# Performance work log

Measured on AMD Instinct MI355X. Metric: run time of the kernel, lower is better.

## Reference

```python
import jax, jax.numpy as jnp
import numpy as np

V_PATCH = (1, 2, 4, 8, 16, 32)
RESI = 0.5   # abs(quant_resi)
BETA = 0.25
K_PHI = 4    # share_quant_resi


def _phi_idx(si, SN, K=K_PHI):
    # PhiPartiallyShared.__getitem__ with at = si/(SN-1)
    ticks = np.linspace(1/3/K, 1 - 1/3/K, K) if K == 4 else np.linspace(1/2/K, 1 - 1/2/K, K)
    return int(np.argmin(np.abs(ticks - si / (SN - 1))))


def _area_down(x, pn):
    # F.interpolate mode='area' with pn | H  == exact block mean
    B, C, H, W = x.shape
    return x.reshape(B, C, pn, H // pn, pn, W // pn).mean(axis=(3, 5))


def _bilinear(x, size):
    # matches torch bilinear, align_corners=False, antialias=False (half-pixel centers)
    B, C, _, _ = x.shape
    return jax.image.resize(x, (B, C, size, size), method='bilinear', antialias=False)


def _down(x, pn, si):
    if pn == x.shape[2]:
        return x
    return _area_down(x, pn) if si <= 3 else _bilinear(x, pn)


def _phi_ada(h, w, b, fw, fb, sn):
    # Phi_ada: conv weight modulated by fc(SN); fc is zero-init but kept in the graph
    C = h.shape[1]
    cond = (fw[:, 0] * jnp.float32(sn) + fb).reshape(C, C, 1, 1)
    wmod = w * (1.0 + cond)
    y = jax.lax.conv_general_dilated(h, wmod, (1, 1), 'SAME',
                                     dimension_numbers=('NCHW', 'OIHW', 'NCHW'))
    y = y + b[None, :, None, None]
    return h * (1.0 - RESI) + y * RESI


def _forward(f, embed_w, conv_w, conv_b, fc_w, fc_b):
    B, C, H, W = f.shape
    SN = len(V_PATCH)
    f_ng = jax.lax.stop_gradient(f)
    f_rest = f_ng
    f_hat = jnp.zeros_like(f_ng)
    e_ng = jax.lax.stop_gradient(embed_w)            # embedding.weight.data
    e_sq = jnp.sum(e_ng * e_ng, axis=1)              # [V]
    vq_losses = []
    commit = jnp.float32(0.0)
    for si, pn in enumerate(V_PATCH):
        rest = f_rest if si == SN - 1 else _down(f_rest, pn, si)
        rest_NC = rest.transpose(0, 2, 3, 1).reshape(-1, C)          # [N,C]
        # squared L2 distances to codebook, argmin (non-differentiable)
        d = (jnp.sum(rest_NC * rest_NC, axis=1, keepdims=True)
             + e_sq - 2.0 * (rest_NC @ e_ng.T))                       # [N,V]
        idx = jnp.argmin(d, axis=1)                                   # [N]
        h = embed_w[idx].reshape(B, pn, pn, C).transpose(0, 3, 1, 2)  # [B,C,pn,pn]
        if si != SN - 1:
            h = _bilinear(h, H)
        k = _phi_idx(si, SN)
        h = _phi_ada(h, conv_w[k], conv_b[k], fc_w[k], fc_b[k], SN)
        f_hat = f_hat + h
        f_rest = f_rest - jax.lax.stop_gradient(h)    # grad through f_rest is killed by argmin anyway
        vq_losses.append(jnp.mean((f_hat - f_ng) ** 2))
        fh_ng = jax.lax.stop_gradient(f_hat)
        commit = commit + jnp.mean((_down(fh_ng, pn, si) - _down(f, pn, si)) ** 2) * BETA
    commit = commit / SN
    # straight-through estimator
    f_hat_out = jax.lax.stop_gradient(f_hat) - f_ng + f
    return f_hat_out, jnp.stack(vq_losses), commit


def setup_inputs() -> dict:
    key = jax.random.key(0)
    k1, k2, k3 = jax.random.split(key, 3)
    B, C, H, W = 32, 64, 32, 32
    V = 4096
    f_BChw = jax.random.normal(k1, (B, C, H, W), dtype=jnp.float32)
    embed_w = jax.random.normal(k2, (V, C), dtype=jnp.float32) * 0.5  # trunc_normal std=0.5
    conv_w = jax.random.normal(k3, (K_PHI, C, C, 3, 3), dtype=jnp.float32) * 0.02
    conv_b = jnp.zeros((K_PHI, C), dtype=jnp.float32)
    fc_w = jnp.zeros((K_PHI, C * C, 1), dtype=jnp.float32)  # Phi_ada.fc zero-init
    fc_b = jnp.zeros((K_PHI, C * C), dtype=jnp.float32)
    return {'f_BChw': f_BChw, 'embed_w': embed_w, 'conv_w': conv_w,
            'conv_b': conv_b, 'fc_w': fc_w, 'fc_b': fc_b}


def reference(f_BChw, embed_w, conv_w, conv_b, fc_w, fc_b):
    return _forward(f_BChw, embed_w, conv_w, conv_b, fc_w, fc_b)
```

## Files before the change

### kernel.cpp

```cpp
#include <hip/hip_runtime.h>
#include <cfloat>

#define N_ELEM 2097152
#define TAU 2.0e-2f

typedef short s16x8 __attribute__((ext_vector_type(8)));
typedef float f32x4 __attribute__((ext_vector_type(4)));

__device__ __forceinline__ unsigned short f2bf(float v) {
    unsigned u = __float_as_uint(v);
    u += 0x7FFFu + ((u >> 16) & 1u);
    return (unsigned short)(u >> 16);
}
__device__ __forceinline__ float bf2f(unsigned short h) {
    return __uint_as_float(((unsigned)h) << 16);
}

__device__ __forceinline__ float blockReduceSum(float v) {
    __shared__ float red[4];
    #pragma unroll
    for (int off = 32; off; off >>= 1) v += __shfl_down(v, off, 64);
    int wid = threadIdx.x >> 6, lane = threadIdx.x & 63;
    if (lane == 0) red[wid] = v;
    __syncthreads();
    float r = 0.f;
    if (threadIdx.x == 0) {
        int nw = ((int)blockDim.x + 63) >> 6;
        for (int w = 0; w < nw; ++w) r += red[w];
    }
    __syncthreads();
    return r;
}

__global__ void k_embprep(const float* __restrict__ e, float* __restrict__ hesq,
                          unsigned short* __restrict__ ehiN, unsigned short* __restrict__ eloN) {
    int v = blockIdx.x * 256 + threadIdx.x;
    if (v >= 4096) return;
    const float4* r = (const float4*)(e + (size_t)v * 64);
    float s = 0.f;
    #pragma unroll
    for (int i = 0; i < 16; ++i) {
        float4 a = r[i];
        s += a.x * a.x + a.y * a.y + a.z * a.z + a.w * a.w;
    }
    hesq[v] = 0.5f * s;
    for (int i = 0; i < 64; ++i) {
        float x = e[(size_t)v * 64 + i];
        unsigned short h = f2bf(x);
        ehiN[(size_t)v * 64 + i] = h ^ 0x8000u;
        eloN[(size_t)v * 64 + i] = f2bf(x - bf2f(h)) ^ 0x8000u;
    }
}

__global__ void k_wmod(const float* __restrict__ w, const float* __restrict__ fcw,
                       const float* __restrict__ fcb,
                       unsigned short* __restrict__ wh, unsigned short* __restrict__ wl) {
    int i = blockIdx.x * 256 + threadIdx.x;
    if (i >= 4 * 64 * 64 * 9) return;
    int k = i / (64 * 64 * 9);
    int r = i % (64 * 64 * 9);
    int oi = r / 9;
    int t = r % 9;
    int co = oi >> 6, ci = oi & 63;
    float cond = fcw[k * 4096 + oi] * 6.0f + fcb[k * 4096 + oi];
    float v = w[i] * (1.0f + cond);
    size_t o = ((size_t)(k * 9 + t) * 64 + co) * 64 + ci;
    unsigned short h = f2bf(v);
    wh[o] = h;
    wl[o] = f2bf(v - bf2f(h));
}

__global__ __launch_bounds__(256) void k_down_plane(
        const float* __restrict__ f, const float* __restrict__ fhat,
        float* __restrict__ restnc, unsigned short* __restrict__ dhi,
        unsigned short* __restrict__ dlo, float* __restrict__ cmpPrev, int pn) {
    __shared__ float hs[32][16];
    __shared__ float cr[32][16];
    __shared__ float pm[256];
    int bc = blockIdx.x;
    int c = bc & 63, b = bc >> 6;
    int t = threadIdx.x;
    const float4* fp = (const float4*)(f + (size_t)bc * 1024);
    const float4* hp = (const float4*)(fhat + (size_t)bc * 1024);
    float4 a = fp[t], q = hp[t];
    int r = t >> 3, c4 = t & 7;
    hs[r][c4 * 2]     = (a.x - q.x) + (a.y - q.y);
    hs[r][c4 * 2 + 1] = (a.z - q.z) + (a.w - q.w);
    __syncthreads();
    int cpp = 16 / pn;
    for (int i = t; i < 32 * pn; i += 256) {
        int rr = i / pn, px = i % pn;
        float s = 0.f;
        for (int j = 0; j < cpp; ++j) s += hs[rr][px * cpp + j];
        cr[rr][px] = s;
    }
    __syncthreads();
    int s_ = 32 / pn;
    float inv = 1.0f / (float)(s_ * s_);
    for (int p = t; p < pn * pn; p += 256) {
        int py = p / pn, px = p % pn;
        float s = 0.f;
        for (int j = 0; j < s_; ++j) s += cr[py * s_ + j][px];
        float m = s * inv;
        pm[p] = m;
        int n = (b * pn + py) * pn + px;
        size_t o = (size_t)n * 64 + c;
        unsigned short h = f2bf(m);
        restnc[o] = m;
        dhi[o] = h;
        dlo[o] = f2bf(m - bf2f(h));
    }
    if (pn >= 2) {
        __syncthreads();
        int pnp = pn >> 1;
        float m2 = 0.f;
        for (int p = t; p < pnp * pnp; p += 256) {
            int py = p / pnp, px = p % pnp;
            float mm = 0.25f * (pm[(2 * py) * pn + 2 * px] + pm[(2 * py) * pn + 2 * px + 1]
                              + pm[(2 * py + 1) * pn + 2 * px] + pm[(2 * py + 1) * pn + 2 * px + 1]);
            m2 += mm * mm;
        }
        m2 = blockReduceSum(m2);
        if (t == 0) cmpPrev[blockIdx.x] = m2;
    }
}

__global__ void k_trans_nc(const float* __restrict__ A, const float* __restrict__ Bt,
                           float* __restrict__ dst,
                           unsigned short* __restrict__ dhi, unsigned short* __restrict__ dlo,
                           float* __restrict__ cmp) {
    __shared__ float t[64][65];
    int b = blockIdx.x;
    int p0 = blockIdx.y * 64;
    int lane = threadIdx.x & 63, r4 = threadIdx.x >> 6;
    #pragma unroll
    for (int i = 0; i < 16; ++i) {
        int c = i * 4 + r4;
        size_t g = ((size_t)b * 64 + c) * 1024 + p0 + lane;
        t[c][lane] = A[g] - Bt[g];
    }
    __syncthreads();
    #pragma unroll
    for (int i = 0; i < 16; ++i) {
        int p = i * 4 + r4;
        size_t o = ((size_t)(b * 1024 + p0 + p)) * 64 + lane;
        float v = t[lane][p];
        unsigned short h = f2bf(v);
        dst[o] = v;
        dhi[o] = h;
        dlo[o] = f2bf(v - bf2f(h));
    }
    float m2s = 0.f;
    for (int i = threadIdx.x; i < 1024; i += 256) {
        int c = i & 63, px = i >> 6;
        float m = 0.25f * (t[c][2 * px] + t[c][2 * px + 1] + t[c][32 + 2 * px] + t[c][33 + 2 * px]);
        m2s += m * m;
    }
    m2s = blockReduceSum(m2s);
    if (threadIdx.x == 0) cmp[blockIdx.x * 16 + blockIdx.y] = m2s;
}

__global__ __launch_bounds__(256) void k_vq_mfma(
        const unsigned short* __restrict__ resthi, const unsigned short* __restrict__ restlo,
        const unsigned short* __restrict__ embhiN, const unsigned short* __restrict__ embloN,
        const float* __restrict__ hesq,
        float* __restrict__ m1v_, int* __restrict__ m1i_, float* __restrict__ m2v_,
        int N, int CPS) {
    __shared__ __align__(16) unsigned short lah[64 * 64];
    __shared__ __align__(16) unsigned short lal[64 * 64];
    __shared__ __align__(16) float lq[64];
    int tid = threadIdx.x;
    int lane = tid & 63, wv = tid >> 6;
    int split = blockIdx.y;
    int p0 = blockIdx.x * 128 + wv * 32;
    int cr = lane & 15, oct = lane >> 4;
    int ko8 = oct * 8;
    int ptA = p0 + cr, ptB = p0 + 16 + cr;
    int pA = min(ptA, N - 1), pB = min(ptB, N - 1);

    const unsigned short* ra = resthi + (size_t)pA * 64;
    const unsigned short* la = restlo + (size_t)pA * 64;
    const unsigned short* rb = resthi + (size_t)pB * 64;
    const unsigned short* lb = restlo + (size_t)pB * 64;
    s16x8 bhA0 = *(const s16x8*)(ra + ko8);
    s16x8 bhA1 = *(const s16x8*)(ra + 32 + ko8);
    s16x8 blA0 = *(const s16x8*)(la + ko8);
    s16x8 blA1 = *(const s16x8*)(la + 32 + ko8);
    s16x8 bhB0 = *(const s16x8*)(rb + ko8);
    s16x8 bhB1 = *(const s16x8*)(rb + 32 + ko8);
    s16x8 blB0 = *(const s16x8*)(lb + ko8);
    s16x8 blB1 = *(const s16x8*)(lb + 32 + ko8);

    float m1vA = FLT_MAX, m2vA = FLT_MAX; int m1iA = 0;
    float m1vB = FLT_MAX, m2vB = FLT_MAX; int m1iB = 0;
    int sw = (cr & 7) << 4;

    int cbeg = split * CPS;
    for (int oc = 0; oc < CPS; oc += 64) {
        int cb = cbeg + oc;
        __syncthreads();
        for (int t = tid; t < 512; t += 256) {
            int cc = t >> 3, part = t & 7;
            int bo = (cc * 128 + part * 16) ^ ((cc & 7) << 4);
            *(uint4*)((char*)lah + bo) = *(const uint4*)(embhiN + (size_t)(cb + cc) * 64 + part * 8);
            *(uint4*)((char*)lal + bo) = *(const uint4*)(embloN + (size_t)(cb + cc) * 64 + part * 8);
        }
        if (tid < 64) lq[tid] = hesq[cb + tid];
        __syncthreads();
        #pragma unroll
        for (int sub = 0; sub < 4; ++sub) {
            int rowb = (sub * 16 + cr) * 128;
            s16x8 ah0 = *(const s16x8*)((const char*)lah + ((rowb + ko8 * 2) ^ sw));
            s16x8 ah1 = *(const s16x8*)((const char*)lah + ((rowb + 64 + ko8 * 2) ^ sw));
            s16x8 al0 = *(const s16x8*)((const char*)lal + ((rowb + ko8 * 2) ^ sw));
            s16x8 al1 = *(const s16x8*)((const char*)lal + ((rowb + 64 + ko8 * 2) ^ sw));
            f32x4 q = *(const f32x4*)(lq + sub * 16 + oct * 4);
            int crow = cb + sub * 16 + oct * 4;
            f32x4 acc = q;
            acc = __builtin_amdgcn_mfma_f32_16x16x32_bf16(ah0, bhA0, acc, 0, 0, 0);
            acc = __builtin_amdgcn_mfma_f32_16x16x32_bf16(ah1, bhA1, acc, 0, 0, 0);
            acc = __builtin_amdgcn_mfma_f32_16x16x32_bf16(ah0, blA0, acc, 0, 0, 0);
            acc = __builtin_amdgcn_mfma_f32_16x16x32_bf16(ah1, blA1, acc, 0, 0, 0);
            acc = __builtin_amdgcn_mfma_f32_16x16x32_bf16(al0, bhA0, acc, 0, 0, 0);
            acc = __builtin_amdgcn_mfma_f32_16x16x32_bf16(al1, bhA1, acc, 0, 0, 0);
            #pragma unroll
            for (int r = 0; r < 4; ++r) {
                float s = acc[r];
                bool lt = s < m1vA;
                m2vA = fminf(fmaxf(s, m1vA), m2vA);
                m1iA = lt ? (crow + r) : m1iA;
                m1vA = fminf(s, m1vA);
            }
            f32x4 accB = q;
            accB = __builtin_amdgcn_mfma_f32_16x16x32_bf16(ah0, bhB0, accB, 0, 0, 0);
            accB = __builtin_amdgcn_mfma_f32_16x16x32_bf16(ah1, bhB1, accB, 0, 0, 0);
            accB = __builtin_amdgcn_mfma_f32_16x16x32_bf16(ah0, blB0, accB, 0, 0, 0);
            accB = __builtin_amdgcn_mfma_f32_16x16x32_bf16(ah1, blB1, accB, 0, 0, 0);
            accB = __builtin_amdgcn_mfma_f32_16x16x32_bf16(al0, bhB0, accB, 0, 0, 0);
            accB = __builtin_amdgcn_mfma_f32_16x16x32_bf16(al1, bhB1, accB, 0, 0, 0);
            #pragma unroll
            for (int r = 0; r < 4; ++r) {
                float s = accB[r];
                bool lt = s < m1vB;
                m2vB = fminf(fmaxf(s, m1vB), m2vB);
                m1iB = lt ? (crow + r) : m1iB;
                m1vB = fminf(s, m1vB);
            }
        }
    }
    #pragma unroll
    for (int off = 16; off <= 32; off <<= 1) {
        float o1 = __shfl_xor(m1vA, off, 64); int oi = __shfl_xor(m1iA, off, 64);
        float o2 = __shfl_xor(m2vA, off, 64);
        bool lt = o1 < m1vA;
        m2vA = fminf(fmaxf(o1, m1vA), fminf(m2vA, o2));
        m1vA = fminf(o1, m1vA);
        m1iA = lt ? oi : m1iA;
        o1 = __shfl_xor(m1vB, off, 64); oi = __shfl_xor(m1iB, off, 64);
        o2 = __shfl_xor(m2vB, off, 64);
        lt = o1 < m1vB;
        m2vB = fminf(fmaxf(o1, m1vB), fminf(m2vB, o2));
        m1vB = fminf(o1, m1vB);
        m1iB = lt ? oi : m1iB;
    }
    if (oct == 0) {
        if (ptA < N) { size_t o = (size_t)split * N + ptA; m1v_[o] = m1vA; m1i_[o] = m1iA; m2v_[o] = m2vA; }
        if (ptB < N) { size_t o = (size_t)split * N + ptB; m1v_[o] = m1vB; m1i_[o] = m1iB; m2v_[o] = m2vB; }
    }
}

__global__ void k_vq_combine(const float* __restrict__ m1v_, const int* __restrict__ m1i_,
                             const float* __restrict__ m2v_,
                             int* __restrict__ idx, int* __restrict__ flag, int* __restrict__ count,
                             unsigned long long* __restrict__ pmin, int N, int SPLITS) {
    int n = blockIdx.x * 256 + threadIdx.x;
    if (n >= N) return;
    float a1v = m1v_[n], a2v = m2v_[n];
    int a1i = m1i_[n];
    for (int s = 1; s < SPLITS; ++s) {
        size_t o = (size_t)s * N + n;
        float b1v = m1v_[o], b2v = m2v_[o];
        int b1i = m1i_[o];
        bool lt = b1v < a1v;
        a2v = fminf(fmaxf(b1v, a1v), fminf(a2v, b2v));
        a1v = fminf(b1v, a1v);
        a1i = lt ? b1i : a1i;
    }
    idx[n] = a1i;
    pmin[n] = 0xFFFFFFFFFFFFFFFFull;
    if (a2v - a1v < TAU) {
        int p = atomicAdd(count, 1);
        flag[p] = n;
    }
}

__global__ __launch_bounds__(256) void k_vq_exact(
        const float* __restrict__ restnc, const float* __restrict__ embed,
        const float* __restrict__ hesq, const int* __restrict__ flag,
        const int* __restrict__ count, unsigned long long* __restrict__ pmin) {
    __shared__ float rs[32 * 64];
    int tid = threadIdx.x;
    int lane = tid & 63;
    int cnt = *count;
    int nb = (cnt + 31) >> 5;
    int ntask = nb * 16;
    for (int task = blockIdx.x; task < ntask; task += gridDim.x) {
        int batch = task >> 4, spl = task & 15;
        int lbase = batch << 5;
        int npts = min(32, cnt - lbase);
        __syncthreads();
        for (int i = tid; i < npts * 64; i += 256) {
            int li = i >> 6;
            rs[i] = restnc[(size_t)flag[lbase + li] * 64 + (i & 63)];
        }
        __syncthreads();
        int code = spl * 256 + tid;
        const float4* e4 = (const float4*)(embed + (size_t)code * 64);
        float4 e[16];
        #pragma unroll
        for (int i = 0; i < 16; ++i) e[i] = e4[i];
        float hq = hesq[code];
        for (int p = 0; p < npts; ++p) {
            const float4* r4 = (const float4*)(rs + p * 64);
            float d0 = 0.f, d1 = 0.f, d2 = 0.f, d3 = 0.f;
            #pragma unroll
            for (int i = 0; i < 16; i += 4) {
                float4 e0 = e[i], e1 = e[i + 1], e2 = e[i + 2], e3 = e[i + 3];
                d0 += e0.x * r4[i].x     + e0.y * r4[i].y     + e0.z * r4[i].z     + e0.w * r4[i].w;
                d1 += e1.x * r4[i + 1].x + e1.y * r4[i + 1].y + e1.z * r4[i + 1].z + e1.w * r4[i + 1].w;
                d2 += e2.x * r4[i + 2].x + e2.y * r4[i + 2].y + e2.z * r4[i + 2].z + e2.w * r4[i + 2].w;
                d3 += e3.x * r4[i + 3].x + e3.y * r4[i + 3].y + e3.z * r4[i + 3].z + e3.w * r4[i + 3].w;
            }
            float s = hq - ((d0 + d1) + (d2 + d3));
            unsigned u = __float_as_uint(s);
            u = (u & 0x80000000u) ? ~u : (u | 0x80000000u);
            unsigned long long pk = (((unsigned long long)u) << 32) | (unsigned)code;
            #pragma unroll
            for (int off = 32; off; off >>= 1) {
                unsigned long long o = __shfl_down(pk, off, 64);
                if (o < pk) pk = o;
            }
            if (lane == 0) atomicMin(pmin + flag[lbase + p], pk);
        }
    }
}

__global__ __launch_bounds__(256) void k_conv_mfma(
        const int* __restrict__ idx, const unsigned long long* __restrict__ pmin,
        const float* __restrict__ embed,
        const unsigned short* __restrict__ wh, const unsigned short* __restrict__ wl,
        const float* __restrict__ bias, const float* __restrict__ f_in,
        float* __restrict__ f_hat, float* __restrict__ vq_part, int pn) {
    __shared__ __align__(16) unsigned short Xh[4 * 34 * 64];
    __shared__ __align__(16) unsigned short Xl[4 * 34 * 64];
    __shared__ int pid[136][4];
    __shared__ float pwt[136][2];
    int b = blockIdx.x, rg = blockIdx.y;
    int y0 = rg * 2;
    int tid = threadIdx.x;
    int lane = tid & 63, wv = tid >> 6;
    int coh = (wv & 1) * 32;
    int ph  = (wv >> 1) * 2;
    int cr = lane & 15, oct = lane >> 4;

    if (tid < 136) {
        int lr = tid / 34, lc = tid % 34;
        int gy = y0 + lr - 1, gx = lc - 1;
        if (gy >= 0 && gy < 32 && gx >= 0 && gx < 32) {
            if (pn == 32) {
                int n = (b * 32 + gy) * 32 + gx;
                unsigned long long pv = pmin[n];
                int id = (pv != 0xFFFFFFFFFFFFFFFFull) ? (int)(pv & 0xFFFFFFFFull) : idx[n];
                pid[tid][0] = id; pid[tid][1] = id; pid[tid][2] = id; pid[tid][3] = id;
                pwt[tid][0] = 0.f; pwt[tid][1] = 0.f;
            } else {
                float scale = (float)pn * (1.0f / 32.0f);
                float sy = (gy + 0.5f) * scale - 0.5f;
                float sx = (gx + 0.5f) * scale - 0.5f;
                float fy0 = floorf(sy), fx0 = floorf(sx);
                float wy = sy - fy0, wx = sx - fx0;
                int yy0 = max(0, min(pn - 1, (int)fy0));
                int yy1 = max(0, min(pn - 1, (int)fy0 + 1));
                int xx0 = max(0, min(pn - 1, (int)fx0));
                int xx1 = max(0, min(pn - 1, (int)fx0 + 1));
                int nb_ = b * pn * pn;
                int n00 = nb_ + yy0 * pn + xx0, n01 = nb_ + yy0 * pn + xx1;
                int n10 = nb_ + yy1 * pn + xx0, n11 = nb_ + yy1 * pn + xx1;
                unsigned long long p00 = pmin[n00], p01 = pmin[n01];
                unsigned long long p10 = pmin[n10], p11 = pmin[n11];
                pid[tid][0] = (p00 != 0xFFFFFFFFFFFFFFFFull) ? (int)(p00 & 0xFFFFFFFFull) : idx[n00];
                pid[tid][1] = (p01 != 0xFFFFFFFFFFFFFFFFull) ? (int)(p01 & 0xFFFFFFFFull) : idx[n01];
                pid[tid][2] = (p10 != 0xFFFFFFFFFFFFFFFFull) ? (int)(p10 & 0xFFFFFFFFull) : idx[n10];
                pid[tid][3] = (p11 != 0xFFFFFFFFFFFFFFFFull) ? (int)(p11 & 0xFFFFFFFFull) : idx[n11];
                pwt[tid][0] = wy; pwt[tid][1] = wx;
            }
        } else {
            pid[tid][0] = -1;
        }
    }
    __syncthreads();

    for (int q = tid; q < 136 * 8; q += 256) {
        int pl = q >> 3, o8 = q & 7;
        int lc = pl % 34;
        int bo = (pl * 128 + o8 * 16) ^ ((lc & 7) << 4);
        uint4 vh = {0, 0, 0, 0}, vl = {0, 0, 0, 0};
        int i00 = pid[pl][0];
        if (i00 >= 0) {
            int i01 = pid[pl][1], i10 = pid[pl][2], i11 = pid[pl][3];
            float wy = pwt[pl][0], wx = pwt[pl][1];
            const float4* e00 = (const float4*)(embed + (size_t)i00 * 64 + o8 * 8);
            const float4* e01 = (const float4*)(embed + (size_t)i01 * 64 + o8 * 8);
            const float4* e10 = (const float4*)(embed + (size_t)i10 * 64 + o8 * 8);
            const float4* e11 = (const float4*)(embed + (size_t)i11 * 64 + o8 * 8);
            union { unsigned short u[8]; uint4 v; } oh, ol;
            #pragma unroll
            for (int half = 0; half < 2; ++half) {
                float4 a00 = e00[half], a01 = e01[half], a10 = e10[half], a11 = e11[half];
                float vv[4];
                vv[0] = (a00.x + wx * (a01.x - a00.x)) + wy * ((a10.x + wx * (a11.x - a10.x)) - (a00.x + wx * (a01.x - a00.x)));
                vv[1] = (a00.y + wx * (a01.y - a00.y)) + wy * ((a10.y + wx * (a11.y - a10.y)) - (a00.y + wx * (a01.y - a00.y)));
                vv[2] = (a00.z + wx * (a01.z - a00.z)) + wy * ((a10.z + wx * (a11.z - a10.z)) - (a00.z + wx * (a01.z - a00.z)));
                vv[3] = (a00.w + wx * (a01.w - a00.w)) + wy * ((a10.w + wx * (a11.w - a10.w)) - (a00.w + wx * (a01.w - a00.w)));
                #pragma unroll
                for (int j = 0; j < 4; ++j) {
                    unsigned short h = f2bf(vv[j]);
                    oh.u[half * 4 + j] = h;
                    ol.u[half * 4 + j] = f2bf(vv[j] - bf2f(h));
                }
            }
            vh = oh.v; vl = ol.v;
        }
        *(uint4*)((char*)Xh + bo) = vh;
        *(uint4*)((char*)Xl + bo) = vl;
    }
    __syncthreads();

    f32x4 acc[2][2];
    #pragma unroll
    for (int ct = 0; ct < 2; ++ct)
        #pragma unroll
        for (int pp = 0; pp < 2; ++pp) acc[ct][pp] = (f32x4){0.f, 0.f, 0.f, 0.f};

    for (int t = 0; t < 9; ++t) {
        int dy = t / 3, dx = t % 3;
        #pragma unroll
        for (int cc = 0; cc < 2; ++cc) {
            size_t wo0 = ((size_t)t * 64 + coh + cr) * 64 + cc * 32 + oct * 8;
            size_t wo1 = ((size_t)t * 64 + coh + 16 + cr) * 64 + cc * 32 + oct * 8;
            s16x8 Ah0 = *(const s16x8*)(wh + wo0);
            s16x8 Al0 = *(const s16x8*)(wl + wo0);
            s16x8 Ah1 = *(const s16x8*)(wh + wo1);
            s16x8 Al1 = *(const s16x8*)(wl + wo1);
            #pragma unroll
            for (int pp = 0; pp < 2; ++pp) {
                int px = (ph + pp) * 16 + cr;
                int lr = (px >> 5) + dy;
                int lc = (px & 31) + dx;
                int bo = ((lr * 34 + lc) * 128 + cc * 64 + oct * 16) ^ ((lc & 7) << 4);
                s16x8 Bh = *(const s16x8*)((const char*)Xh + bo);
                s16x8 Bl = *(const s16x8*)((const char*)Xl + bo);
                acc[0][pp] = __builtin_amdgcn_mfma_f32_16x16x32_bf16(Ah0, Bh, acc[0][pp], 0, 0, 0);
                acc[0][pp] = __builtin_amdgcn_mfma_f32_16x16x32_bf16(Ah0, Bl, acc[0][pp], 0, 0, 0);
                acc[0][pp] = __builtin_amdgcn_mfma_f32_16x16x32_bf16(Al0, Bh, acc[0][pp], 0, 0, 0);
                acc[1][pp] = __builtin_amdgcn_mfma_f32_16x16x32_bf16(Ah1, Bh, acc[1][pp], 0, 0, 0);
                acc[1][pp] = __builtin_amdgcn_mfma_f32_16x16x32_bf16(Ah1, Bl, acc[1][pp], 0, 0, 0);
                acc[1][pp] = __builtin_amdgcn_mfma_f32_16x16x32_bf16(Al1, Bh, acc[1][pp], 0, 0, 0);
            }
        }
    }

    float local = 0.f;
    #pragma unroll
    for (int ct = 0; ct < 2; ++ct) {
        int cbase = coh + ct * 16 + oct * 4;
        #pragma unroll
        for (int pp = 0; pp < 2; ++pp) {
            int px = (ph + pp) * 16 + cr;
            int y = y0 + (px >> 5), x = px & 31;
            int lr = (px >> 5) + 1, lc = (px & 31) + 1;
            int bo = ((lr * 34 + lc) * 128 + cbase * 2) ^ ((lc & 7) << 4);
            ushort4 hvh = *(const ushort4*)((const char*)Xh + bo);
            ushort4 hvl = *(const ushort4*)((const char*)Xl + bo);
            #pragma unroll
            for (int r = 0; r < 4; ++r) {
                int co = cbase + r;
                unsigned short uh = (r == 0) ? hvh.x : (r == 1) ? hvh.y : (r == 2) ? hvh.z : hvh.w;
                unsigned short ul = (r == 0) ? hvl.x : (r == 1) ? hvl.y : (r == 2) ? hvl.z : hvl.w;
                float hv = bf2f(uh) + bf2f(ul);
                float hconv = acc[ct][pp][r] + bias[co];
                float hout = 0.5f * hv + 0.5f * hconv;
                size_t o = (((size_t)(b * 64 + co)) * 32 + y) * 32 + x;
                float fh = f_hat[o] + hout;
                f_hat[o] = fh;
                float d = fh - f_in[o];
                local += d * d;
            }
        }
    }
    local = blockReduceSum(local);
    if (tid == 0) vq_part[b * 16 + rg] = local;
}

__global__ void k_final(const float* __restrict__ vqp, const float* __restrict__ cmpP,
                        float* __restrict__ out) {
    const int pn2s[5] = {1, 4, 16, 64, 256};
    const int slots[5] = {2048, 2048, 2048, 2048, 512};
    __shared__ float commit_s;
    if (threadIdx.x == 0) commit_s = 0.f;
    __syncthreads();
    for (int si = 0; si < 6; ++si) {
        float l = vqp[si * 512 + threadIdx.x] + vqp[si * 512 + 256 + threadIdx.x];
        l = blockReduceSum(l);
        if (threadIdx.x == 0) {
            float vl = l / (float)N_ELEM;
            out[N_ELEM + si] = vl;
            if (si == 5) commit_s += vl * 0.25f;
        }
        if (si < 5) {
            float csum = 0.f;
            for (int i = threadIdx.x; i < slots[si]; i += 256) csum += cmpP[si * 2048 + i];
            csum = blockReduceSum(csum);
            if (threadIdx.x == 0) commit_s += csum / (float)(2048 * pn2s[si]) * 0.25f;
        }
    }
    __syncthreads();
    if (threadIdx.x == 0) out[N_ELEM + 6] = commit_s / 6.0f;
}

extern "C" void kernel_launch(void* const* d_in, const int* in_sizes, int n_in,
                              void* d_out, int out_size, void* d_ws, size_t ws_size,
                              hipStream_t stream) {
    const float* f     = (const float*)d_in[0];
    const float* embed = (const float*)d_in[1];
    const float* convw = (const float*)d_in[2];
    const float* convb = (const float*)d_in[3];
    const float* fcw   = (const float*)d_in[4];
    const float* fcb   = (const float*)d_in[5];
    float* out = (float*)d_out;
    float* ws  = (float*)d_ws;

    float* restnc = ws + 2097152;
    unsigned short* resthi = (unsigned short*)(ws + 4194304);
    unsigned short* restlo = (unsigned short*)(ws + 5242880);
    unsigned short* embhiN = (unsigned short*)(ws + 6291456);
    unsigned short* embloN = (unsigned short*)(ws + 6422528);
    unsigned short* wmodh  = (unsigned short*)(ws + 6553600);
    unsigned short* wmodl  = (unsigned short*)(ws + 6627328);
    float* hesq   = ws + 6701056;
    float* m1v    = ws + 6705152;
    float* m2v    = ws + 6967296;
    int*   m1i    = (int*)(ws + 7229440);
    int*   idx    = (int*)(ws + 7491584);
    int*   flag   = (int*)(ws + 7524352);
    int*   count  = (int*)(ws + 7557120);
    unsigned long long* pmin = (unsigned long long*)(ws + 7557184);
    float* vqp    = ws + 7622720;
    float* cmpP   = ws + 7625792;

    hipMemsetAsync(d_out, 0, (size_t)out_size * sizeof(float), stream);
    hipMemsetAsync(count, 0, 6 * sizeof(int), stream);
    k_wmod<<<576, 256, 0, stream>>>(convw, fcw, fcb, wmodh, wmodl);
    k_embprep<<<16, 256, 0, stream>>>(embed, hesq, embhiN, embloN);

    const int pns[6]    = {1, 2, 4, 8, 16, 32};
    const int splits[6] = {64, 64, 64, 64, 16, 8};
    const int kidx[6]   = {0, 0, 1, 2, 3, 3};

    for (int si = 0; si < 6; ++si) {
        int pn = pns[si], pn2 = pn * pn;
        int N = 32 * pn2, SPL = splits[si], CPS = 4096 / SPL;

        if (si <= 4) {
            k_down_plane<<<2048, 256, 0, stream>>>(f, out, restnc, resthi, restlo,
                                                   si >= 1 ? cmpP + (si - 1) * 2048 : nullptr, pn);
        } else {
            k_trans_nc<<<dim3(32, 16), 256, 0, stream>>>(f, out, restnc, resthi, restlo,
                                                         cmpP + 4 * 2048);
        }

        k_vq_mfma<<<dim3((N + 127) / 128, SPL), 256, 0, stream>>>(resthi, restlo, embhiN, embloN, hesq,
                                                                  m1v, m1i, m2v, N, CPS);
        k_vq_combine<<<(N + 255) / 256, 256, 0, stream>>>(m1v, m1i, m2v, idx, flag, count + si, pmin, N, SPL);
        k_vq_exact<<<512, 256, 0, stream>>>(restnc, embed, hesq, flag, count + si, pmin);

        k_conv_mfma<<<dim3(32, 16), 256, 0, stream>>>(idx, pmin, embed,
                                                      wmodh + kidx[si] * 36864, wmodl + kidx[si] * 36864,
                                                      convb + kidx[si] * 64, f, out, vqp + si * 512, pn);
    }

    k_final<<<1, 256, 0, stream>>>(vqp, cmpP, out);
}
```

Baseline: 609.9 us.

## Enlarge conv tile to four rows per block and fold count reset into prep

The conv kernel now processes four output rows per block with 512 threads and a six-row halo tile instead of two rows with 256 threads. This halves the halo overhead and halves the block count. The pn==32 path skips the redundant four-way bilinear gather, and the count memset is folded into k_embprep to save a launch. The wave-to-row mapping must extend to eight waves. The larger LDS footprint and block size may reduce occupancy.

```diff
diff --git a/kernel.cpp b/kernel.cpp
--- a/kernel.cpp
+++ b/kernel.cpp
@@ -17,7 +17,7 @@
 }
 
 __device__ __forceinline__ float blockReduceSum(float v) {
-    __shared__ float red[4];
+    __shared__ float red[8];
     #pragma unroll
     for (int off = 32; off; off >>= 1) v += __shfl_down(v, off, 64);
     int wid = threadIdx.x >> 6, lane = threadIdx.x & 63;
@@ -33,7 +33,9 @@
 }
 
 __global__ void k_embprep(const float* __restrict__ e, float* __restrict__ hesq,
-                          unsigned short* __restrict__ ehiN, unsigned short* __restrict__ eloN) {
+                          unsigned short* __restrict__ ehiN, unsigned short* __restrict__ eloN,
+                          int* __restrict__ count) {
+    if (blockIdx.x == 0 && threadIdx.x < 6) count[threadIdx.x] = 0;
     int v = blockIdx.x * 256 + threadIdx.x;
     if (v >= 4096) return;
     const float4* r = (const float4*)(e + (size_t)v * 64);
@@ -345,25 +347,25 @@
     }
 }
 
-__global__ __launch_bounds__(256) void k_conv_mfma(
+__global__ __launch_bounds__(512) void k_conv_mfma(
         const int* __restrict__ idx, const unsigned long long* __restrict__ pmin,
         const float* __restrict__ embed,
         const unsigned short* __restrict__ wh, const unsigned short* __restrict__ wl,
         const float* __restrict__ bias, const float* __restrict__ f_in,
         float* __restrict__ f_hat, float* __restrict__ vq_part, int pn) {
-    __shared__ __align__(16) unsigned short Xh[4 * 34 * 64];
-    __shared__ __align__(16) unsigned short Xl[4 * 34 * 64];
-    __shared__ int pid[136][4];
-    __shared__ float pwt[136][2];
+    __shared__ __align__(16) unsigned short Xh[6 * 34 * 64];
+    __shared__ __align__(16) unsigned short Xl[6 * 34 * 64];
+    __shared__ int pid[204][4];
+    __shared__ float pwt[204][2];
     int b = blockIdx.x, rg = blockIdx.y;
-    int y0 = rg * 2;
+    int y0 = rg * 4;
     int tid = threadIdx.x;
     int lane = tid & 63, wv = tid >> 6;
     int coh = (wv & 1) * 32;
     int ph  = (wv >> 1) * 2;
     int cr = lane & 15, oct = lane >> 4;
 
-    if (tid < 136) {
+    if (tid < 204) {
         int lr = tid / 34, lc = tid % 34;
         int gy = y0 + lr - 1, gx = lc - 1;
         if (gy >= 0 && gy < 32 && gx >= 0 && gx < 32) {
@@ -371,8 +373,7 @@
                 int n = (b * 32 + gy) * 32 + gx;
                 unsigned long long pv = pmin[n];
                 int id = (pv != 0xFFFFFFFFFFFFFFFFull) ? (int)(pv & 0xFFFFFFFFull) : idx[n];
-                pid[tid][0] = id; pid[tid][1] = id; pid[tid][2] = id; pid[tid][3] = id;
-                pwt[tid][0] = 0.f; pwt[tid][1] = 0.f;
+                pid[tid][0] = id;
             } else {
                 float scale = (float)pn * (1.0f / 32.0f);
                 float sy = (gy + 0.5f) * scale - 0.5f;
@@ -400,33 +401,48 @@
     }
     __syncthreads();
 
-    for (int q = tid; q < 136 * 8; q += 256) {
+    for (int q = tid; q < 204 * 8; q += 512) {
         int pl = q >> 3, o8 = q & 7;
         int lc = pl % 34;
         int bo = (pl * 128 + o8 * 16) ^ ((lc & 7) << 4);
         uint4 vh = {0, 0, 0, 0}, vl = {0, 0, 0, 0};
         int i00 = pid[pl][0];
         if (i00 >= 0) {
-            int i01 = pid[pl][1], i10 = pid[pl][2], i11 = pid[pl][3];
-            float wy = pwt[pl][0], wx = pwt[pl][1];
-            const float4* e00 = (const float4*)(embed + (size_t)i00 * 64 + o8 * 8);
-            const float4* e01 = (const float4*)(embed + (size_t)i01 * 64 + o8 * 8);
-            const float4* e10 = (const float4*)(embed + (size_t)i10 * 64 + o8 * 8);
-            const float4* e11 = (const float4*)(embed + (size_t)i11 * 64 + o8 * 8);
             union { unsigned short u[8]; uint4 v; } oh, ol;
-            #pragma unroll
-            for (int half = 0; half < 2; ++half) {
-                float4 a00 = e00[half], a01 = e01[half], a10 = e10[half], a11 = e11[half];
-                float vv[4];
-                vv[0] = (a00.x + wx * (a01.x - a00.x)) + wy * ((a10.x + wx * (a11.x - a10.x)) - (a00.x + wx * (a01.x - a00.x)));
-                vv[1] = (a00.y + wx * (a01.y - a00.y)) + wy * ((a10.y + wx * (a11.y - a10.y)) - (a00.y + wx * (a01.y - a00.y)));
-                vv[2] = (a00.z + wx * (a01.z - a00.z)) + wy * ((a10.z + wx * (a11.z - a10.z)) - (a00.z + wx * (a01.z - a00.z)));
-                vv[3] = (a00.w + wx * (a01.w - a00.w)) + wy * ((a10.w + wx * (a11.w - a10.w)) - (a00.w + wx * (a01.w - a00.w)));
+            if (pn == 32) {
+                const float4* e00 = (const float4*)(embed + (size_t)i00 * 64 + o8 * 8);
                 #pragma unroll
-                for (int j = 0; j < 4; ++j) {
-                    unsigned short h = f2bf(vv[j]);
-                    oh.u[half * 4 + j] = h;
-                    ol.u[half * 4 + j] = f2bf(vv[j] - bf2f(h));
+                for (int half = 0; half < 2; ++half) {
+                    float4 a00 = e00[half];
+                    float vv[4] = {a00.x, a00.y, a00.z, a00.w};
+                    #pragma unroll
+                    for (int j = 0; j < 4; ++j) {
+                        unsigned short h = f2bf(vv[j]);
+                        oh.u[half * 4 + j] = h;
+                        ol.u[half * 4 + j] = f2bf(vv[j] - bf2f(h));
+                    }
+                }
+            } else {
+                int i01 = pid[pl][1], i10 = pid[pl][2], i11 = pid[pl][3];
+                float wy = pwt[pl][0], wx = pwt[pl][1];
+                const float4* e00 = (const float4*)(embed + (size_t)i00 * 64 + o8 * 8);
+                const float4* e01 = (const float4*)(embed + (size_t)i01 * 64 + o8 * 8);
+                const float4* e10 = (const float4*)(embed + (size_t)i10 * 64 + o8 * 8);
+                const float4* e11 = (const float4*)(embed + (size_t)i11 * 64 + o8 * 8);
+                #pragma unroll
+                for (int half = 0; half < 2; ++half) {
+                    float4 a00 = e00[half], a01 = e01[half], a10 = e10[half], a11 = e11[half];
+                    float t0, t1, vv[4];
+                    t0 = a00.x + wx * (a01.x - a00.x); t1 = a10.x + wx * (a11.x - a10.x); vv[0] = t0 + wy * (t1 - t0);
+                    t0 = a00.y + wx * (a01.y - a00.y); t1 = a10.y + wx * (a11.y - a10.y); vv[1] = t0 + wy * (t1 - t0);
+                    t0 = a00.z + wx * (a01.z - a00.z); t1 = a10.z + wx * (a11.z - a10.z); vv[2] = t0 + wy * (t1 - t0);
+                    t0 = a00.w + wx * (a01.w - a00.w); t1 = a10.w + wx * (a11.w - a10.w); vv[3] = t0 + wy * (t1 - t0);
+                    #pragma unroll
+                    for (int j = 0; j < 4; ++j) {
+                        unsigned short h = f2bf(vv[j]);
+                        oh.u[half * 4 + j] = h;
+                        ol.u[half * 4 + j] = f2bf(vv[j] - bf2f(h));
+                    }
                 }
             }
             vh = oh.v; vl = ol.v;
@@ -499,7 +515,7 @@
         }
     }
     local = blockReduceSum(local);
-    if (tid == 0) vq_part[b * 16 + rg] = local;
+    if (tid == 0) vq_part[b * 8 + rg] = local;
 }
 
 __global__ void k_final(const float* __restrict__ vqp, const float* __restrict__ cmpP,
@@ -510,7 +526,7 @@
     if (threadIdx.x == 0) commit_s = 0.f;
     __syncthreads();
     for (int si = 0; si < 6; ++si) {
-        float l = vqp[si * 512 + threadIdx.x] + vqp[si * 512 + 256 + threadIdx.x];
+        float l = vqp[si * 256 + threadIdx.x];
         l = blockReduceSum(l);
         if (threadIdx.x == 0) {
             float vl = l / (float)N_ELEM;
@@ -556,12 +572,11 @@
     int*   count  = (int*)(ws + 7557120);
     unsigned long long* pmin = (unsigned long long*)(ws + 7557184);
     float* vqp    = ws + 7622720;
-    float* cmpP   = ws + 7625792;
+    float* cmpP   = ws + 7624256;
 
     hipMemsetAsync(d_out, 0, (size_t)out_size * sizeof(float), stream);
-    hipMemsetAsync(count, 0, 6 * sizeof(int), stream);
     k_wmod<<<576, 256, 0, stream>>>(convw, fcw, fcb, wmodh, wmodl);
-    k_embprep<<<16, 256, 0, stream>>>(embed, hesq, embhiN, embloN);
+    k_embprep<<<16, 256, 0, stream>>>(embed, hesq, embhiN, embloN, count);
 
     const int pns[6]    = {1, 2, 4, 8, 16, 32};
     const int splits[6] = {64, 64, 64, 64, 16, 8};
@@ -584,9 +599,9 @@
         k_vq_combine<<<(N + 255) / 256, 256, 0, stream>>>(m1v, m1i, m2v, idx, flag, count + si, pmin, N, SPL);
         k_vq_exact<<<512, 256, 0, stream>>>(restnc, embed, hesq, flag, count + si, pmin);
 
-        k_conv_mfma<<<dim3(32, 16), 256, 0, stream>>>(idx, pmin, embed,
-                                                      wmodh + kidx[si] * 36864, wmodl + kidx[si] * 36864,
-                                                      convb + kidx[si] * 64, f, out, vqp + si * 512, pn);
+        k_conv_mfma<<<dim3(32, 8), 512, 0, stream>>>(idx, pmin, embed,
+                                                     wmodh + kidx[si] * 36864, wmodl + kidx[si] * 36864,
+                                                     convb + kidx[si] * 64, f, out, vqp + si * 256, pn);
     }
 
     k_final<<<1, 256, 0, stream>>>(vqp, cmpP, out);
```

Result: faster. 587.1 us (-3.7%).
